# Performance work log

Hardware: AMD Instinct MI355X
Metric: run time of the kernel (lower is better)

The kernel has to match this reference:

```python
import jax, jax.numpy as jnp
import numpy as np

E = 64      # hidden_dim
FF = 128    # ff_dim
H = 4       # nhead
D = E // H  # head_dim = 16
STEPS = 16  # recursion_steps
IN = 200    # input_dim
B = 131072  # batch


def _ln(h, g, b):
    m = h.mean(-1, keepdims=True)
    v = ((h - m) ** 2).mean(-1, keepdims=True)
    return (h - m) * jax.lax.rsqrt(v + 1e-5) * g + b


def _ffn(h, w1, b1, w2, b2):
    return jax.nn.gelu(h @ w1.T + b1, approximate=False) @ w2.T + b2


def _forward(x, W_in, b_in, g_in, be_in,
             z_in_w, z_in_b, z_out_w, z_out_b,
             z_ffn_w1, z_ffn_b1, z_ffn_w2, z_ffn_b2,
             zn1_g, zn1_b, zn2_g, zn2_b,
             y_in_w, y_in_b, y_out_w, y_out_b,
             y_ffn_w1, y_ffn_b1, y_ffn_w2, y_ffn_b2,
             yn1_g, yn1_b, yn2_g, yn2_b,
             W_out, b_out):
    Bn = x.shape[0]
    x_proj = jax.nn.gelu(_ln(x @ W_in.T + b_in, g_in, be_in), approximate=False)  # [B,E]
    y0 = jnp.zeros((Bn, E), dtype=x.dtype)
    z0 = jnp.zeros((Bn, E), dtype=x.dtype)
    scale = 1.0 / np.sqrt(D).astype(np.float32)
    Wv_y = y_in_w[2 * E:]   # cross-attn over a single kv token: softmax weight == 1,
    bv_y = y_in_b[2 * E:]   # so output = out_proj(v_proj(z)) exactly (no approximation)

    def step(carry, _):
        y, z = carry
        seq = jnp.stack([x_proj, y, z], axis=1)            # [B,3,E]
        qkv = seq @ z_in_w.T + z_in_b                      # [B,3,3E]
        q, k, v = jnp.split(qkv, 3, axis=-1)
        rh = lambda t: t.reshape(Bn, 3, H, D).transpose(0, 2, 1, 3)  # [B,H,3,D]
        q, k, v = rh(q), rh(k), rh(v)
        att = jax.nn.softmax(jnp.einsum('bhsd,bhtd->bhst', q, k) * scale, axis=-1)
        o = jnp.einsum('bhst,bhtd->bhsd', att, v).transpose(0, 2, 1, 3).reshape(Bn, 3, E)
        o = o @ z_out_w.T + z_out_b
        z_res = _ln(z + o[:, 2, :], zn1_g, zn1_b)
        z2 = _ln(z_res + _ffn(z_res, z_ffn_w1, z_ffn_b1, z_ffn_w2, z_ffn_b2), zn2_g, zn2_b)
        ca = (z2 @ Wv_y.T + bv_y) @ y_out_w.T + y_out_b    # 1-token cross-attention
        y_res = _ln(y + ca, yn1_g, yn1_b)
        y2 = _ln(y_res + _ffn(y_res, y_ffn_w1, y_ffn_b1, y_ffn_w2, y_ffn_b2), yn2_g, yn2_b)
        return (y2, z2), None

    (y, z), _ = jax.lax.scan(step, (y0, z0), None, length=STEPS)
    return (y @ W_out.T + b_out)[:, 0]                     # [B]


def setup_inputs() -> dict:
    key = jax.random.key(0)
    ks = jax.random.split(key, 12)
    f = lambda k, s: jax.random.normal(k, s, dtype=jnp.float32) * 0.05
    zeros = lambda s: jnp.zeros(s, dtype=jnp.float32)
    ones = lambda s: jnp.ones(s, dtype=jnp.float32)
    return {
        'x': jax.random.normal(ks[0], (B, IN), dtype=jnp.float32),
        'W_in': f(ks[1], (E, IN)), 'b_in': zeros((E,)),
        'g_in': ones((E,)), 'be_in': zeros((E,)),
        'z_in_w': f(ks[2], (3 * E, E)), 'z_in_b': zeros((3 * E,)),
        'z_out_w': f(ks[3], (E, E)), 'z_out_b': zeros((E,)),
        'z_ffn_w1': f(ks[4], (FF, E)), 'z_ffn_b1': zeros((FF,)),
        'z_ffn_w2': f(ks[5], (E, FF)), 'z_ffn_b2': zeros((E,)),
        'zn1_g': ones((E,)), 'zn1_b': zeros((E,)),
        'zn2_g': ones((E,)), 'zn2_b': zeros((E,)),
        'y_in_w': f(ks[6], (3 * E, E)), 'y_in_b': zeros((3 * E,)),
        'y_out_w': f(ks[7], (E, E)), 'y_out_b': zeros((E,)),
        'y_ffn_w1': f(ks[8], (FF, E)), 'y_ffn_b1': zeros((FF,)),
        'y_ffn_w2': f(ks[9], (E, FF)), 'y_ffn_b2': zeros((E,)),
        'yn1_g': ones((E,)), 'yn1_b': zeros((E,)),
        'yn2_g': ones((E,)), 'yn2_b': zeros((E,)),
        'W_out': f(ks[10], (1, E)), 'b_out': zeros((1,)),
    }


def reference(x, W_in, b_in, g_in, be_in,
              z_in_w, z_in_b, z_out_w, z_out_b,
              z_ffn_w1, z_ffn_b1, z_ffn_w2, z_ffn_b2,
              zn1_g, zn1_b, zn2_g, zn2_b,
              y_in_w, y_in_b, y_out_w, y_out_b,
              y_ffn_w1, y_ffn_b1, y_ffn_w2, y_ffn_b2,
              yn1_g, yn1_b, yn2_g, yn2_b,
              W_out, b_out):
    return _forward(x, W_in, b_in, g_in, be_in,
                    z_in_w, z_in_b, z_out_w, z_out_b,
                    z_ffn_w1, z_ffn_b1, z_ffn_w2, z_ffn_b2,
                    zn1_g, zn1_b, zn2_g, zn2_b,
                    y_in_w, y_in_b, y_out_w, y_out_b,
                    y_ffn_w1, y_ffn_b1, y_ffn_w2, y_ffn_b2,
                    yn1_g, yn1_b, yn2_g, yn2_b,
                    W_out, b_out)
```

## Files before the change

### kernel.cpp

```cpp
#include <hip/hip_runtime.h>
#include <math.h>


constexpr int STEPS = 16;
constexpr int INDIM = 200;

typedef __attribute__((ext_vector_type(8))) short bfrag8;
typedef __attribute__((ext_vector_type(4))) float f32x4;
typedef __attribute__((ext_vector_type(4))) short s16x4;

constexpr int FB_WIN  = 0;
constexpr int NFRAG   = 140;
constexpr int NPARAM  = 1544;

constexpr int LB_ZQ   = 0;
constexpr int LB_ZK   = 8;
constexpr int LB_ZV   = 16;
constexpr int LB_ZOUT = 24;
constexpr int LB_ZF1  = 32;
constexpr int LB_ZF2  = 48;
constexpr int LB_YV   = 64;
constexpr int LB_YOUT = 72;
constexpr int LB_YF1  = 80;
constexpr int LB_YF2  = 96;
constexpr int NSTEADY = 112;

constexpr int PB_BIN   = 0;
constexpr int PB_GIN   = 64;
constexpr int PB_BEIN  = 128;
constexpr int PB_ZINB  = 192;
constexpr int PB_ZOUTB = 384;
constexpr int PB_ZF1B  = 448;
constexpr int PB_ZF2B  = 576;
constexpr int PB_ZN1G  = 640;
constexpr int PB_ZN1B  = 704;
constexpr int PB_ZN2G  = 768;
constexpr int PB_ZN2B  = 832;
constexpr int PB_YVB   = 896;
constexpr int PB_YOUTB = 960;
constexpr int PB_YF1B  = 1024;
constexpr int PB_YF2B  = 1152;
constexpr int PB_YN1G  = 1216;
constexpr int PB_YN1B  = 1280;
constexpr int PB_YN2G  = 1344;
constexpr int PB_YN2B  = 1408;
constexpr int PB_WOUT  = 1472;
constexpr int PB_BOUT  = 1536;

constexpr int S64      = 72;
constexpr int L_W      = 0;
constexpr int L_P      = 57344;
constexpr int L_ACT    = 60432;
constexpr int WAVE_SH  = 1152;
constexpr int NWAVE    = 16;
constexpr int ARENA_SH = L_ACT + NWAVE * WAVE_SH;

struct Params {
  const float *x, *W_in, *b_in, *g_in, *be_in;
  const float *z_in_w, *z_in_b, *z_out_w, *z_out_b;
  const float *z_ffn_w1, *z_ffn_b1, *z_ffn_w2, *z_ffn_b2;
  const float *zn1_g, *zn1_b, *zn2_g, *zn2_b;
  const float *y_in_w, *y_in_b, *y_out_w, *y_out_b;
  const float *y_ffn_w1, *y_ffn_b1, *y_ffn_w2, *y_ffn_b2;
  const float *yn1_g, *yn1_b, *yn2_g, *yn2_b;
  const float *W_out, *b_out;
  float *out;
  int nrows;
};

__device__ __forceinline__ ushort f2bf(float f) {
  uint u = __float_as_uint(f);
  u += 0x7FFFu + ((u >> 16) & 1u);
  return (ushort)(u >> 16);
}
__device__ __forceinline__ uint pk2(float a, float b) {
  return (uint)f2bf(a) | ((uint)f2bf(b) << 16);
}
__device__ __forceinline__ float upk_lo(uint u) {
  return __uint_as_float(u << 16);
}
__device__ __forceinline__ float upk_hi(uint u) {
  return __uint_as_float(u & 0xFFFF0000u);
}
__device__ __forceinline__ float dot4(f32x4 a, f32x4 b) {
  return a.x * b.x + a.y * b.y + a.z * b.z + a.w * b.w;
}
__device__ __forceinline__ void stc(short* buf, int stride, int mt, int q,
                                    int s, f32x4 c) {
  s16x4 v;
  v.x = (short)f2bf(c.x); v.y = (short)f2bf(c.y);
  v.z = (short)f2bf(c.z); v.w = (short)f2bf(c.w);
  *(s16x4*)(buf + s * stride + mt * 16 + q * 4) = v;
}

__device__ __forceinline__ void c2b_p(const uint p[8], bfrag8& b0, bfrag8& b1,
                                      int lane) {
  const int srcA = (lane & 15) | ((lane & 16) << 1);
  const int srcB = srcA + 16;
  const bool odd = (lane & 32) != 0;
  uint ev0 = p[0], ev1 = p[1], ev2 = p[4], ev3 = p[5];
  uint od0 = p[2], od1 = p[3], od2 = p[6], od3 = p[7];
  uint rA0, rA1, rA2, rA3, rB0, rB1, rB2, rB3;
  {
    uint e, o;
    e = (uint)__shfl((int)ev0, srcA); o = (uint)__shfl((int)od0, srcA); rA0 = odd ? o : e;
    e = (uint)__shfl((int)ev1, srcA); o = (uint)__shfl((int)od1, srcA); rA1 = odd ? o : e;
    e = (uint)__shfl((int)ev2, srcA); o = (uint)__shfl((int)od2, srcA); rA2 = odd ? o : e;
    e = (uint)__shfl((int)ev3, srcA); o = (uint)__shfl((int)od3, srcA); rA3 = odd ? o : e;
    e = (uint)__shfl((int)ev0, srcB); o = (uint)__shfl((int)od0, srcB); rB0 = odd ? o : e;
    e = (uint)__shfl((int)ev1, srcB); o = (uint)__shfl((int)od1, srcB); rB1 = odd ? o : e;
    e = (uint)__shfl((int)ev2, srcB); o = (uint)__shfl((int)od2, srcB); rB2 = odd ? o : e;
    e = (uint)__shfl((int)ev3, srcB); o = (uint)__shfl((int)od3, srcB); rB3 = odd ? o : e;
  }
  union U { uint u[4]; bfrag8 b; };
  U u0, u1;
  u0.u[0] = rA0; u0.u[1] = rA1; u0.u[2] = rB0; u0.u[3] = rB1;
  u1.u[0] = rA2; u1.u[1] = rA3; u1.u[2] = rB2; u1.u[3] = rB3;
  b0 = u0.b; b1 = u1.b;
}
__device__ __forceinline__ void c2b(const f32x4 c[4], bfrag8& b0, bfrag8& b1,
                                    int lane) {
  uint p[8];
#pragma unroll
  for (int mt = 0; mt < 4; ++mt) {
    p[2 * mt]     = pk2(c[mt].x, c[mt].y);
    p[2 * mt + 1] = pk2(c[mt].z, c[mt].w);
  }
  c2b_p(p, b0, b1, lane);
}

template <int MT>
__device__ __forceinline__ void layerN(const short* in, const short* lw,
                                       int fbase, const float* bias, f32x4* c,
                                       int lane, int q, int s) {
  bfrag8 bf[2];
#pragma unroll
  for (int kt = 0; kt < 2; ++kt)
    bf[kt] = *(const bfrag8*)(in + s * S64 + kt * 32 + q * 8);
#pragma unroll
  for (int mt = 0; mt < MT; ++mt)
    c[mt] = *(const f32x4*)(bias + mt * 16 + q * 4);
#pragma unroll
  for (int mt = 0; mt < MT; ++mt) {
#pragma unroll
    for (int kt = 0; kt < 2; ++kt) {
      bfrag8 af = *(const bfrag8*)(lw + (fbase + mt * 2 + kt) * 512 + lane * 8);
      c[mt] = __builtin_amdgcn_mfma_f32_16x16x32_bf16(af, bf[kt], c[mt], 0, 0, 0);
    }
  }
}

template <int MT, int KT>
__device__ __forceinline__ void layerBK(const bfrag8* bf, const short* lw,
                                        int fbase, const float* bias, f32x4* c,
                                        int lane, int q) {
#pragma unroll
  for (int mt = 0; mt < MT; ++mt)
    c[mt] = *(const f32x4*)(bias + mt * 16 + q * 4);
#pragma unroll
  for (int mt = 0; mt < MT; ++mt) {
#pragma unroll
    for (int kt = 0; kt < KT; ++kt) {
      bfrag8 af = *(const bfrag8*)(lw + (fbase + mt * KT + kt) * 512 + lane * 8);
      c[mt] = __builtin_amdgcn_mfma_f32_16x16x32_bf16(af, bf[kt], c[mt], 0, 0, 0);
    }
  }
}

template <int MT>
__device__ __forceinline__ void layerB2(const bfrag8* bfA, const bfrag8* bfB,
                                        const short* lw, int fbase,
                                        const float* bias, f32x4* cA, f32x4* cB,
                                        int lane, int q) {
#pragma unroll
  for (int mt = 0; mt < MT; ++mt) {
    f32x4 b4 = *(const f32x4*)(bias + mt * 16 + q * 4);
    cA[mt] = b4; cB[mt] = b4;
  }
#pragma unroll
  for (int mt = 0; mt < MT; ++mt) {
#pragma unroll
    for (int kt = 0; kt < 2; ++kt) {
      bfrag8 af = *(const bfrag8*)(lw + (fbase + mt * 2 + kt) * 512 + lane * 8);
      cA[mt] = __builtin_amdgcn_mfma_f32_16x16x32_bf16(af, bfA[kt], cA[mt], 0, 0, 0);
      cB[mt] = __builtin_amdgcn_mfma_f32_16x16x32_bf16(af, bfB[kt], cB[mt], 0, 0, 0);
    }
  }
}

__device__ __forceinline__ void lnorm_c(f32x4 c[4], const float* g,
                                        const float* b, int q) {
  float sm = 0.f;
#pragma unroll
  for (int mt = 0; mt < 4; ++mt) sm += c[mt].x + c[mt].y + c[mt].z + c[mt].w;
  sm += __shfl_xor(sm, 16); sm += __shfl_xor(sm, 32);
  float mean = sm * (1.f / 64.f);
  float vs = 0.f;
#pragma unroll
  for (int mt = 0; mt < 4; ++mt) {
    f32x4 d = c[mt];
    d.x -= mean; d.y -= mean; d.z -= mean; d.w -= mean;
    c[mt] = d;
    vs += d.x * d.x + d.y * d.y + d.z * d.z + d.w * d.w;
  }
  vs += __shfl_xor(vs, 16); vs += __shfl_xor(vs, 32);
  float rs = rsqrtf(vs * (1.f / 64.f) + 1e-5f);
#pragma unroll
  for (int mt = 0; mt < 4; ++mt) {
    f32x4 g4 = *(const f32x4*)(g + mt * 16 + q * 4);
    f32x4 b4 = *(const f32x4*)(b + mt * 16 + q * 4);
    f32x4 v = c[mt];
    v.x = v.x * rs * g4.x + b4.x; v.y = v.y * rs * g4.y + b4.y;
    v.z = v.z * rs * g4.z + b4.z; v.w = v.w * rs * g4.w + b4.w;
    c[mt] = v;
  }
}

__device__ __forceinline__ float gelu1(float x) {
  float ax = fabsf(x) * 0.70710678118654752f;
  float t = __builtin_amdgcn_rcpf(1.0f + 0.3275911f * ax);
  float poly =
      ((((1.061405429f * t - 1.453152027f) * t + 1.421413741f) * t -
        0.284496736f) * t + 0.254829592f) * t;
  float e = __expf(-ax * ax);
  float erfv = copysignf(1.0f - poly * e, x);
  return 0.5f * x * (1.0f + erfv);
}

__global__ void prepack_kernel(Params p, ushort* wf) {
  int f = blockIdx.x;
  int lane = threadIdx.x;

  if (f == NFRAG) {
    float* pw = (float*)(wf + (size_t)NFRAG * 512);
    for (int t = lane; t < NPARAM; t += 64) {
      float v = 0.f;
      if      (t < 64)   v = p.b_in[t];
      else if (t < 128)  v = p.g_in[t - 64];
      else if (t < 192)  v = p.be_in[t - 128];
      else if (t < 384)  v = p.z_in_b[t - 192];
      else if (t < 448)  v = p.z_out_b[t - 384];
      else if (t < 576)  v = p.z_ffn_b1[t - 448];
      else if (t < 640)  v = p.z_ffn_b2[t - 576];
      else if (t < 704)  v = p.zn1_g[t - 640];
      else if (t < 768)  v = p.zn1_b[t - 704];
      else if (t < 832)  v = p.zn2_g[t - 768];
      else if (t < 896)  v = p.zn2_b[t - 832];
      else if (t < 960)  v = p.y_in_b[128 + t - 896];
      else if (t < 1024) v = p.y_out_b[t - 960];
      else if (t < 1152) v = p.y_ffn_b1[t - 1024];
      else if (t < 1216) v = p.y_ffn_b2[t - 1152];
      else if (t < 1280) v = p.yn1_g[t - 1216];
      else if (t < 1344) v = p.yn1_b[t - 1280];
      else if (t < 1408) v = p.yn2_g[t - 1344];
      else if (t < 1472) v = p.yn2_b[t - 1408];
      else if (t < 1536) v = p.W_out[t - 1472];
      else if (t == 1536) v = p.b_out[0];
      pw[t] = v;
    }
    return;
  }

  int q = lane >> 4, r = lane & 15;
  const float* src; int K, mt, kt, l;
  if (f < 28)        { src = p.W_in;                K = 200; mt = f / 7;  kt = f % 7; }
  else if (f < 36)   { l = f - 28;  src = p.z_in_w;            K = 64;  mt = l / 2; kt = l % 2; }
  else if (f < 44)   { l = f - 36;  src = p.z_in_w + 64 * 64;  K = 64;  mt = l / 2; kt = l % 2; }
  else if (f < 52)   { l = f - 44;  src = p.z_in_w + 128 * 64; K = 64;  mt = l / 2; kt = l % 2; }
  else if (f < 60)   { l = f - 52;  src = p.z_out_w;           K = 64;  mt = l / 2; kt = l % 2; }
  else if (f < 76)   { l = f - 60;  src = p.z_ffn_w1;          K = 64;  mt = l / 2; kt = l % 2; }
  else if (f < 92)   { l = f - 76;  src = p.z_ffn_w2;          K = 128; mt = l / 4; kt = l % 4; }
  else if (f < 100)  { l = f - 92;  src = p.y_in_w + 128 * 64; K = 64;  mt = l / 2; kt = l % 2; }
  else if (f < 108)  { l = f - 100; src = p.y_out_w;           K = 64;  mt = l / 2; kt = l % 2; }
  else if (f < 124)  { l = f - 108; src = p.y_ffn_w1;          K = 64;  mt = l / 2; kt = l % 2; }
  else               { l = f - 124; src = p.y_ffn_w2;          K = 128; mt = l / 4; kt = l % 4; }

  int row = mt * 16 + r;
  int col = kt * 32 + q * 8;
  bfrag8 o;
#pragma unroll
  for (int j = 0; j < 8; ++j) {
    int cc = col + j;
    float v = (cc < K) ? src[(size_t)row * K + cc] : 0.0f;
    o[j] = (short)f2bf(v);
  }
  *(bfrag8*)(wf + (size_t)f * 512 + lane * 8) = o;
}

__global__ __launch_bounds__(1024, 1)
void trm_mfma_kernel(Params p, const ushort* wf) {
  __shared__ __align__(16) short arena[ARENA_SH];
  const int tid = threadIdx.x;
  const int wave = tid >> 6, lane = tid & 63;
  const int q = lane >> 4, s = lane & 15;

  {
    const uint4* srcw = (const uint4*)(wf + (size_t)28 * 512);
    uint4* dstw = (uint4*)(arena + L_W);
    for (int i = tid; i < NSTEADY * 64; i += 1024) dstw[i] = srcw[i];
    const uint4* srcp = (const uint4*)(wf + (size_t)NFRAG * 512);
    uint4* dstp = (uint4*)(arena + L_P);
    for (int i = tid; i < NPARAM / 4; i += 1024) dstp[i] = srcp[i];
  }
  __syncthreads();

  const short* LW = arena + L_W;
  const float* P  = (const float*)(arena + L_P);
  short* TH = arena + L_ACT + wave * WAVE_SH;

  const int chunks = (p.nrows + 255) / 256;
  for (int ic = blockIdx.x; ic < chunks; ic += gridDim.x) {
    const int row0 = ic * 256 + wave * 16;
    int row = row0 + s;
    if (row >= p.nrows) row = p.nrows - 1;

    bfrag8 xpB[2];
    {
      const float* xr = p.x + (size_t)row * INDIM;
      bfrag8 xb[7];
#pragma unroll
      for (int kt = 0; kt < 7; ++kt) {
        int k0i = kt * 32 + q * 8;
        bfrag8 t;
        if (kt < 6 || q == 0) {
          f32x4 lo = *(const f32x4*)(xr + k0i);
          f32x4 hi = *(const f32x4*)(xr + k0i + 4);
          t[0] = (short)f2bf(lo.x); t[1] = (short)f2bf(lo.y);
          t[2] = (short)f2bf(lo.z); t[3] = (short)f2bf(lo.w);
          t[4] = (short)f2bf(hi.x); t[5] = (short)f2bf(hi.y);
          t[6] = (short)f2bf(hi.z); t[7] = (short)f2bf(hi.w);
        } else {
#pragma unroll
          for (int j = 0; j < 8; ++j) t[j] = 0;
        }
        xb[kt] = t;
      }
      f32x4 c[4];
#pragma unroll
      for (int mt = 0; mt < 4; ++mt)
        c[mt] = *(const f32x4*)(P + PB_BIN + mt * 16 + q * 4);
#pragma unroll
      for (int mt = 0; mt < 4; ++mt)
#pragma unroll
        for (int kt = 0; kt < 7; ++kt) {
          bfrag8 af =
              *(const bfrag8*)(wf + (size_t)(FB_WIN + mt * 7 + kt) * 512 + lane * 8);
          c[mt] = __builtin_amdgcn_mfma_f32_16x16x32_bf16(af, xb[kt], c[mt], 0, 0, 0);
        }
      lnorm_c(c, P + PB_GIN, P + PB_BEIN, q);
#pragma unroll
      for (int mt = 0; mt < 4; ++mt) {
        c[mt].x = gelu1(c[mt].x); c[mt].y = gelu1(c[mt].y);
        c[mt].z = gelu1(c[mt].z); c[mt].w = gelu1(c[mt].w);
      }
      c2b(c, xpB[0], xpB[1], lane);
    }

    uint k0p[8], v0p[8], zCp[8], yCp[8];
    bfrag8 zB[2], yB[2];
    {
      f32x4 ck[4], cv[4];
      layerBK<4, 2>(xpB, LW, LB_ZK, P + PB_ZINB + 64, ck, lane, q);
      layerBK<4, 2>(xpB, LW, LB_ZV, P + PB_ZINB + 128, cv, lane, q);
#pragma unroll
      for (int mt = 0; mt < 4; ++mt) {
        k0p[2 * mt]     = pk2(ck[mt].x, ck[mt].y);
        k0p[2 * mt + 1] = pk2(ck[mt].z, ck[mt].w);
        v0p[2 * mt]     = pk2(cv[mt].x, cv[mt].y);
        v0p[2 * mt + 1] = pk2(cv[mt].z, cv[mt].w);
        zCp[2 * mt] = 0u; zCp[2 * mt + 1] = 0u;
        yCp[2 * mt] = 0u; yCp[2 * mt + 1] = 0u;
      }
#pragma unroll
      for (int kt = 0; kt < 2; ++kt) {
        bfrag8 t;
#pragma unroll
        for (int j = 0; j < 8; ++j) t[j] = 0;
        zB[kt] = t; yB[kt] = t;
      }
    }

    for (int st = 0; st < STEPS; ++st) {
      float w0[4], w1[4], w2[4], wi[4];
      {
        f32x4 q2[4], kz[4], ky[4];
        layerBK<4, 2>(zB, LW, LB_ZQ, P + PB_ZINB, q2, lane, q);
        layerB2<4>(zB, yB, LW, LB_ZK, P + PB_ZINB + 64, kz, ky, lane, q);
#pragma unroll
        for (int mt = 0; mt < 4; ++mt) {
          float a0 = q2[mt].x * upk_lo(k0p[2 * mt]) +
                     q2[mt].y * upk_hi(k0p[2 * mt]) +
                     q2[mt].z * upk_lo(k0p[2 * mt + 1]) +
                     q2[mt].w * upk_hi(k0p[2 * mt + 1]);
          float a1 = dot4(q2[mt], ky[mt]);
          float a2 = dot4(q2[mt], kz[mt]);
          a0 += __shfl_xor(a0, 16); a0 += __shfl_xor(a0, 32);
          a1 += __shfl_xor(a1, 16); a1 += __shfl_xor(a1, 32);
          a2 += __shfl_xor(a2, 16); a2 += __shfl_xor(a2, 32);
          a0 *= 0.25f; a1 *= 0.25f; a2 *= 0.25f;
          float mx = fmaxf(a0, fmaxf(a1, a2));
          float e0 = __expf(a0 - mx), e1 = __expf(a1 - mx), e2 = __expf(a2 - mx);
          w0[mt] = e0; w1[mt] = e1; w2[mt] = e2;
          wi[mt] = __builtin_amdgcn_rcpf(e0 + e1 + e2);
        }
      }
      {
        f32x4 vz[4], vy[4];
        layerB2<4>(zB, yB, LW, LB_ZV, P + PB_ZINB + 128, vz, vy, lane, q);
#pragma unroll
        for (int mt = 0; mt < 4; ++mt) {
          f32x4 o;
          o.x = (upk_lo(v0p[2 * mt])     * w0[mt] + vy[mt].x * w1[mt] +
                 vz[mt].x * w2[mt]) * wi[mt];
          o.y = (upk_hi(v0p[2 * mt])     * w0[mt] + vy[mt].y * w1[mt] +
                 vz[mt].y * w2[mt]) * wi[mt];
          o.z = (upk_lo(v0p[2 * mt + 1]) * w0[mt] + vy[mt].z * w1[mt] +
                 vz[mt].z * w2[mt]) * wi[mt];
          o.w = (upk_hi(v0p[2 * mt + 1]) * w0[mt] + vy[mt].w * w1[mt] +
                 vz[mt].w * w2[mt]) * wi[mt];
          stc(TH, S64, mt, q, s, o);
        }
      }

      uint zrp[8];
      {
        f32x4 zr[4];
        layerN<4>(TH, LW, LB_ZOUT, P + PB_ZOUTB, zr, lane, q, s);
#pragma unroll
        for (int mt = 0; mt < 4; ++mt) {
          zr[mt].x += upk_lo(zCp[2 * mt]);     zr[mt].y += upk_hi(zCp[2 * mt]);
          zr[mt].z += upk_lo(zCp[2 * mt + 1]); zr[mt].w += upk_hi(zCp[2 * mt + 1]);
        }
        lnorm_c(zr, P + PB_ZN1G, P + PB_ZN1B, q);
#pragma unroll
        for (int mt = 0; mt < 4; ++mt) {
          stc(TH, S64, mt, q, s, zr[mt]);
          zrp[2 * mt]     = pk2(zr[mt].x, zr[mt].y);
          zrp[2 * mt + 1] = pk2(zr[mt].z, zr[mt].w);
        }
      }

      bfrag8 hB[4];
      {
        f32x4 h8[8];
        layerN<8>(TH, LW, LB_ZF1, P + PB_ZF1B, h8, lane, q, s);
#pragma unroll
        for (int g = 0; g < 2; ++g) {
          uint ph[8];
#pragma unroll
          for (int mt = 0; mt < 4; ++mt) {
            f32x4 h = h8[4 * g + mt];
            h.x = gelu1(h.x); h.y = gelu1(h.y);
            h.z = gelu1(h.z); h.w = gelu1(h.w);
            ph[2 * mt]     = pk2(h.x, h.y);
            ph[2 * mt + 1] = pk2(h.z, h.w);
          }
          c2b_p(ph, hB[2 * g], hB[2 * g + 1], lane);
        }
      }
      f32x4 z2[4];
      layerBK<4, 4>(hB, LW, LB_ZF2, P + PB_ZF2B, z2, lane, q);
#pragma unroll
      for (int mt = 0; mt < 4; ++mt) {
        z2[mt].x += upk_lo(zrp[2 * mt]);     z2[mt].y += upk_hi(zrp[2 * mt]);
        z2[mt].z += upk_lo(zrp[2 * mt + 1]); z2[mt].w += upk_hi(zrp[2 * mt + 1]);
      }
      lnorm_c(z2, P + PB_ZN2G, P + PB_ZN2B, q);
      {
        uint zp[8];
#pragma unroll
        for (int mt = 0; mt < 4; ++mt) {
          zp[2 * mt]     = pk2(z2[mt].x, z2[mt].y);
          zp[2 * mt + 1] = pk2(z2[mt].z, z2[mt].w);
          zCp[2 * mt] = zp[2 * mt]; zCp[2 * mt + 1] = zp[2 * mt + 1];
        }
        c2b_p(zp, zB[0], zB[1], lane);
      }

      f32x4 t4[4];
      layerBK<4, 2>(zB, LW, LB_YV, P + PB_YVB, t4, lane, q);
#pragma unroll
      for (int mt = 0; mt < 4; ++mt) stc(TH, S64, mt, q, s, t4[mt]);

      uint yrp[8];
      {
        f32x4 yr[4];
        layerN<4>(TH, LW, LB_YOUT, P + PB_YOUTB, yr, lane, q, s);
#pragma unroll
        for (int mt = 0; mt < 4; ++mt) {
          yr[mt].x += upk_lo(yCp[2 * mt]);     yr[mt].y += upk_hi(yCp[2 * mt]);
          yr[mt].z += upk_lo(yCp[2 * mt + 1]); yr[mt].w += upk_hi(yCp[2 * mt + 1]);
        }
        lnorm_c(yr, P + PB_YN1G, P + PB_YN1B, q);
#pragma unroll
        for (int mt = 0; mt < 4; ++mt) {
          stc(TH, S64, mt, q, s, yr[mt]);
          yrp[2 * mt]     = pk2(yr[mt].x, yr[mt].y);
          yrp[2 * mt + 1] = pk2(yr[mt].z, yr[mt].w);
        }
      }

      {
        f32x4 h8[8];
        layerN<8>(TH, LW, LB_YF1, P + PB_YF1B, h8, lane, q, s);
#pragma unroll
        for (int g = 0; g < 2; ++g) {
          uint ph[8];
#pragma unroll
          for (int mt = 0; mt < 4; ++mt) {
            f32x4 h = h8[4 * g + mt];
            h.x = gelu1(h.x); h.y = gelu1(h.y);
            h.z = gelu1(h.z); h.w = gelu1(h.w);
            ph[2 * mt]     = pk2(h.x, h.y);
            ph[2 * mt + 1] = pk2(h.z, h.w);
          }
          c2b_p(ph, hB[2 * g], hB[2 * g + 1], lane);
        }
      }
      f32x4 y2[4];
      layerBK<4, 4>(hB, LW, LB_YF2, P + PB_YF2B, y2, lane, q);
#pragma unroll
      for (int mt = 0; mt < 4; ++mt) {
        y2[mt].x += upk_lo(yrp[2 * mt]);     y2[mt].y += upk_hi(yrp[2 * mt]);
        y2[mt].z += upk_lo(yrp[2 * mt + 1]); y2[mt].w += upk_hi(yrp[2 * mt + 1]);
      }
      lnorm_c(y2, P + PB_YN2G, P + PB_YN2B, q);
      {
        uint yp[8];
#pragma unroll
        for (int mt = 0; mt < 4; ++mt) {
          yp[2 * mt]     = pk2(y2[mt].x, y2[mt].y);
          yp[2 * mt + 1] = pk2(y2[mt].z, y2[mt].w);
          yCp[2 * mt] = yp[2 * mt]; yCp[2 * mt + 1] = yp[2 * mt + 1];
        }
        c2b_p(yp, yB[0], yB[1], lane);
      }
    }

    float acc = 0.f;
#pragma unroll
    for (int mt = 0; mt < 4; ++mt) {
      f32x4 w4 = *(const f32x4*)(P + PB_WOUT + mt * 16 + q * 4);
      acc += upk_lo(yCp[2 * mt]) * w4.x + upk_hi(yCp[2 * mt]) * w4.y +
             upk_lo(yCp[2 * mt + 1]) * w4.z + upk_hi(yCp[2 * mt + 1]) * w4.w;
    }
    acc += __shfl_xor(acc, 16); acc += __shfl_xor(acc, 32);
    if (q == 0 && (row0 + s) < p.nrows) p.out[row0 + s] = acc + P[PB_BOUT];
  }
}

extern "C" void kernel_launch(void* const* d_in, const int* in_sizes, int n_in,
                              void* d_out, int out_size, void* d_ws,
                              size_t ws_size, hipStream_t stream) {
  Params p;
  const float* const* in = (const float* const*)d_in;
  p.x        = in[0];  p.W_in     = in[1];  p.b_in     = in[2];
  p.g_in     = in[3];  p.be_in    = in[4];
  p.z_in_w   = in[5];  p.z_in_b   = in[6];
  p.z_out_w  = in[7];  p.z_out_b  = in[8];
  p.z_ffn_w1 = in[9];  p.z_ffn_b1 = in[10];
  p.z_ffn_w2 = in[11]; p.z_ffn_b2 = in[12];
  p.zn1_g    = in[13]; p.zn1_b    = in[14];
  p.zn2_g    = in[15]; p.zn2_b    = in[16];
  p.y_in_w   = in[17]; p.y_in_b   = in[18];
  p.y_out_w  = in[19]; p.y_out_b  = in[20];
  p.y_ffn_w1 = in[21]; p.y_ffn_b1 = in[22];
  p.y_ffn_w2 = in[23]; p.y_ffn_b2 = in[24];
  p.yn1_g    = in[25]; p.yn1_b    = in[26];
  p.yn2_g    = in[27]; p.yn2_b    = in[28];
  p.W_out    = in[29]; p.b_out    = in[30];
  p.out      = (float*)d_out;
  p.nrows    = in_sizes[0] / INDIM;

  if (ws_size < (size_t)NFRAG * 1024 + NPARAM * 4) return;
  ushort* wf = (ushort*)d_ws;

  hipLaunchKernelGGL(prepack_kernel, dim3(NFRAG + 1), dim3(64), 0, stream, p, wf);
  hipLaunchKernelGGL(trm_mfma_kernel, dim3(256), dim3(1024), 0, stream, p, wf);
}
```

Baseline: 957.1 us.

## Shrink blocks to 12 waves, split FFN1 into halves, launch one block per chunk

Cuts waves per block from 16 to 12, which reduces the block's register-file footprint and lets each wave keep more VGPRs under launch_bounds. The FFN first layer is now computed in two 64-wide halves, so only four accumulator tiles are live at once instead of eight, lowering register pressure. The grid is sized to the number of row chunks (682 blocks) instead of a fixed 256 persistent blocks. The trade-off is that each block reloads the shared weights from global memory, and the extra blocks add tail imbalance across CUs.

Result: slower. 1.093 ms (+14.2%).

```diff
diff --git a/kernel.cpp b/kernel.cpp
--- a/kernel.cpp
+++ b/kernel.cpp
@@ -52,8 +52,11 @@
 constexpr int L_P      = 57344;
 constexpr int L_ACT    = 60432;
 constexpr int WAVE_SH  = 1152;
-constexpr int NWAVE    = 16;
+constexpr int NWAVE    = 12;
 constexpr int ARENA_SH = L_ACT + NWAVE * WAVE_SH;
+
+constexpr int BLK      = 64 * NWAVE;
+constexpr int ROWS_PB  = 16 * NWAVE;
 
 struct Params {
   const float *x, *W_in, *b_in, *g_in, *be_in;
@@ -287,7 +290,7 @@
   *(bfrag8*)(wf + (size_t)f * 512 + lane * 8) = o;
 }
 
-__global__ __launch_bounds__(1024, 1)
+__global__ __launch_bounds__(BLK, 1)
 void trm_mfma_kernel(Params p, const ushort* wf) {
   __shared__ __align__(16) short arena[ARENA_SH];
   const int tid = threadIdx.x;
@@ -297,10 +300,10 @@
   {
     const uint4* srcw = (const uint4*)(wf + (size_t)28 * 512);
     uint4* dstw = (uint4*)(arena + L_W);
-    for (int i = tid; i < NSTEADY * 64; i += 1024) dstw[i] = srcw[i];
+    for (int i = tid; i < NSTEADY * 64; i += BLK) dstw[i] = srcw[i];
     const uint4* srcp = (const uint4*)(wf + (size_t)NFRAG * 512);
     uint4* dstp = (uint4*)(arena + L_P);
-    for (int i = tid; i < NPARAM / 4; i += 1024) dstp[i] = srcp[i];
+    for (int i = tid; i < NPARAM / 4; i += BLK) dstp[i] = srcp[i];
   }
   __syncthreads();
 
@@ -308,9 +311,9 @@
   const float* P  = (const float*)(arena + L_P);
   short* TH = arena + L_ACT + wave * WAVE_SH;
 
-  const int chunks = (p.nrows + 255) / 256;
+  const int chunks = (p.nrows + ROWS_PB - 1) / ROWS_PB;
   for (int ic = blockIdx.x; ic < chunks; ic += gridDim.x) {
-    const int row0 = ic * 256 + wave * 16;
+    const int row0 = ic * ROWS_PB + wave * 16;
     int row = row0 + s;
     if (row >= p.nrows) row = p.nrows - 1;
 
@@ -441,22 +444,19 @@
       }
 
       bfrag8 hB[4];
-      {
-        f32x4 h8[8];
-        layerN<8>(TH, LW, LB_ZF1, P + PB_ZF1B, h8, lane, q, s);
-#pragma unroll
-        for (int g = 0; g < 2; ++g) {
-          uint ph[8];
-#pragma unroll
-          for (int mt = 0; mt < 4; ++mt) {
-            f32x4 h = h8[4 * g + mt];
-            h.x = gelu1(h.x); h.y = gelu1(h.y);
-            h.z = gelu1(h.z); h.w = gelu1(h.w);
-            ph[2 * mt]     = pk2(h.x, h.y);
-            ph[2 * mt + 1] = pk2(h.z, h.w);
-          }
-          c2b_p(ph, hB[2 * g], hB[2 * g + 1], lane);
-        }
+#pragma unroll
+      for (int g = 0; g < 2; ++g) {
+        f32x4 h4[4];
+        layerN<4>(TH, LW, LB_ZF1 + 8 * g, P + PB_ZF1B + 64 * g, h4, lane, q, s);
+        uint ph[8];
+#pragma unroll
+        for (int mt = 0; mt < 4; ++mt) {
+          h4[mt].x = gelu1(h4[mt].x); h4[mt].y = gelu1(h4[mt].y);
+          h4[mt].z = gelu1(h4[mt].z); h4[mt].w = gelu1(h4[mt].w);
+          ph[2 * mt]     = pk2(h4[mt].x, h4[mt].y);
+          ph[2 * mt + 1] = pk2(h4[mt].z, h4[mt].w);
+        }
+        c2b_p(ph, hB[2 * g], hB[2 * g + 1], lane);
       }
       f32x4 z2[4];
       layerBK<4, 4>(hB, LW, LB_ZF2, P + PB_ZF2B, z2, lane, q);
@@ -500,22 +500,19 @@
         }
       }
 
-      {
-        f32x4 h8[8];
-        layerN<8>(TH, LW, LB_YF1, P + PB_YF1B, h8, lane, q, s);
-#pragma unroll
-        for (int g = 0; g < 2; ++g) {
-          uint ph[8];
-#pragma unroll
-          for (int mt = 0; mt < 4; ++mt) {
-            f32x4 h = h8[4 * g + mt];
-            h.x = gelu1(h.x); h.y = gelu1(h.y);
-            h.z = gelu1(h.z); h.w = gelu1(h.w);
-            ph[2 * mt]     = pk2(h.x, h.y);
-            ph[2 * mt + 1] = pk2(h.z, h.w);
-          }
-          c2b_p(ph, hB[2 * g], hB[2 * g + 1], lane);
-        }
+#pragma unroll
+      for (int g = 0; g < 2; ++g) {
+        f32x4 h4[4];
+        layerN<4>(TH, LW, LB_YF1 + 8 * g, P + PB_YF1B + 64 * g, h4, lane, q, s);
+        uint ph[8];
+#pragma unroll
+        for (int mt = 0; mt < 4; ++mt) {
+          h4[mt].x = gelu1(h4[mt].x); h4[mt].y = gelu1(h4[mt].y);
+          h4[mt].z = gelu1(h4[mt].z); h4[mt].w = gelu1(h4[mt].w);
+          ph[2 * mt]     = pk2(h4[mt].x, h4[mt].y);
+          ph[2 * mt + 1] = pk2(h4[mt].z, h4[mt].w);
+        }
+        c2b_p(ph, hB[2 * g], hB[2 * g + 1], lane);
       }
       f32x4 y2[4];
       layerBK<4, 4>(hB, LW, LB_YF2, P + PB_YF2B, y2, lane, q);
@@ -576,5 +573,6 @@
   ushort* wf = (ushort*)d_ws;
 
   hipLaunchKernelGGL(prepack_kernel, dim3(NFRAG + 1), dim3(64), 0, stream, p, wf);
-  hipLaunchKernelGGL(trm_mfma_kernel, dim3(256), dim3(1024), 0, stream, p, wf);
-}
+  int blocks = (p.nrows + ROWS_PB - 1) / ROWS_PB;
+  hipLaunchKernelGGL(trm_mfma_kernel, dim3(blocks), dim3(BLK), 0, stream, p, wf);
+}
```
